# Kernel optimization log

Hardware: AMD Instinct MI355X
Metric: run time of the kernel (lower is better)

The kernel has to match this reference:

```python
import jax, jax.numpy as jnp
import numpy as np

H = 512   # hidden_size == mm_dim
C = 8     # chunks
R = 8     # rank
S = H // C  # chunk size = 64
OUT = 512 # output_dim of linear_merge
EPS = 1e-12

def _linear(x, w, b):
    # torch nn.Linear convention: w [out, in]
    return x @ w.T + b

def setup_inputs() -> dict:
    key = jax.random.key(0)
    ks = jax.random.split(key, 24)
    B, Lq, Lk, D = 8, 160, 160, 512
    s = 0.02
    inp = {
        'v': jax.random.normal(ks[0], (B, Lk, D), jnp.float32),
        'k': jax.random.normal(ks[1], (B, Lk, D), jnp.float32),
        'q': jax.random.normal(ks[2], (B, Lq, D), jnp.float32),
        # input projections
        'w_v': jax.random.normal(ks[3], (H, D)) * s, 'b_v': jnp.zeros((H,)),
        'w_k': jax.random.normal(ks[4], (H, D)) * s, 'b_k': jnp.zeros((H,)),
        'w_q': jax.random.normal(ks[5], (H, D)) * s, 'b_q': jnp.zeros((H,)),
        # Block: linear0 (applied to key), linear1 (applied to query)
        'w0': jax.random.normal(ks[6], (H, H)) * s, 'b0': jnp.zeros((H,)),
        'w1': jax.random.normal(ks[7], (H, H)) * s, 'b1': jnp.zeros((H,)),
        # per-chunk merge linears, stacked: [C, S*R, S]
        'wm0': jax.random.normal(ks[8], (C, S * R, S)) * s, 'bm0': jnp.zeros((C, S * R)),
        'wm1': jax.random.normal(ks[9], (C, S * R, S)) * s, 'bm1': jnp.zeros((C, S * R)),
        # Block linear_out: mm_dim -> 1
        'w_bo': jax.random.normal(ks[10], (1, H)) * s, 'b_bo': jnp.zeros((1,)),
        # linear_merge: hidden -> output_dim
        'w_m': jax.random.normal(ks[11], (OUT, H)) * s, 'b_m': jnp.zeros((OUT,)),
    }
    return inp

def _block_scores(kx, qx, w0, b0, w1, b1, wm0, bm0, wm1, bm1, w_bo, b_bo):
    # kx: [B,Lk,H] (block arg 0 = key), qx: [B,Lq,H] (block arg 1 = query)
    x0 = _linear(kx, w0, b0)                      # [B,Lk,H]
    x1 = _linear(qx, w1, b1)                      # [B,Lq,H]
    B_, Lk = x0.shape[0], x0.shape[1]
    Lq = x1.shape[1]
    x0c = x0.reshape(B_, Lk, C, S)
    x1c = x1.reshape(B_, Lq, C, S)
    # per-chunk merge projections to rank*size
    y0 = jnp.einsum('bkcs,cts->bkct', x0c, wm0) + bm0  # [B,Lk,C,R*S]
    y1 = jnp.einsum('bqcs,cts->bqct', x1c, wm1) + bm1  # [B,Lq,C,R*S]
    y0 = y0.reshape(B_, Lk, C, R, S)
    y1 = y1.reshape(B_, Lq, C, R, S)
    # elementwise product summed over rank, pairwise over (q,k)
    z = jnp.einsum('bqcrs,bkcrs->bqkcs', y1, y0)  # [B,Lq,Lk,C,S]
    # signed sqrt (power norm) then per-chunk L2 normalize
    z = jnp.sqrt(jax.nn.relu(z)) - jnp.sqrt(jax.nn.relu(-z))
    z = z / jnp.maximum(jnp.linalg.norm(z, axis=-1, keepdims=True), EPS)
    z = z.reshape(B_, Lq, Lk, C * S)
    return _linear(z, w_bo, b_bo).squeeze(-1)     # [B,Lq,Lk]

def reference(v, k, q, w_v, b_v, w_k, b_k, w_q, b_q, w0, b0, w1, b1,
              wm0, bm0, wm1, bm1, w_bo, b_bo, w_m, b_m):
    vv = _linear(v, w_v, b_v)   # [B,Lk,H]
    kk = _linear(k, w_k, b_k)   # [B,Lk,H]
    qq = _linear(q, w_q, b_q)   # [B,Lq,H]
    scores = _block_scores(kk, qq, w0, b0, w1, b1, wm0, bm0, wm1, bm1, w_bo, b_bo)
    att = jax.nn.softmax(scores, axis=-1)          # dropout = identity (eval)
    atted = jnp.einsum('bqk,bkh->bqh', att, vv)    # [B,Lq,H]
    B_ = atted.shape[0]
    # faithful to torch: transpose(1,2).contiguous().view(B,-1,H)
    atted = jnp.swapaxes(atted, 1, 2).reshape(B_, -1, H)
    out = _linear(atted, w_m, b_m)                 # [B,Lq,OUT]
    return jnp.squeeze(out)
```

## Files before the change

### kernel.cpp

```cpp
#include <hip/hip_runtime.h>
#include <hip/hip_bf16.h>

#define B_  8
#define LQ  160
#define LK  160

struct GOps {
    const float* A[3];
    const float* W[3];
    const float* Bi[3];
    float*       C[3];
};

__global__ __launch_bounds__(256) void gemm_f(GOps ops, int K)
{
    const int op = blockIdx.z;
    const float* __restrict__ A  = ops.A[op];
    const float* __restrict__ W  = ops.W[op];
    const float* __restrict__ Bi = ops.Bi[op];
    float* __restrict__       C  = ops.C[op];

    const int m0 = blockIdx.y << 6;
    const int n0 = blockIdx.x << 6;
    const int tid = threadIdx.x;
    const int tm  = tid >> 4;
    const int tn  = tid & 15;
    const int lr  = tid >> 2;
    const int lk4 = (tid & 3) << 2;

    __shared__ float As[16][64];
    __shared__ float Ws[16][64];

    float acc[4][4];
#pragma unroll
    for (int i = 0; i < 4; i++)
#pragma unroll
        for (int j = 0; j < 4; j++) acc[i][j] = 0.f;

    const float* Arow = A + (long)(m0 + lr) * 512 + lk4;
    const float* Wrow = W + (long)(n0 + lr) * K + lk4;
    float4 av = *(const float4*)(Arow);
    float4 wv = *(const float4*)(Wrow);

    for (int k0 = 0; k0 < K; k0 += 16) {
        __syncthreads();
        As[lk4 + 0][lr] = av.x; As[lk4 + 1][lr] = av.y;
        As[lk4 + 2][lr] = av.z; As[lk4 + 3][lr] = av.w;
        Ws[lk4 + 0][lr] = wv.x; Ws[lk4 + 1][lr] = wv.y;
        Ws[lk4 + 2][lr] = wv.z; Ws[lk4 + 3][lr] = wv.w;
        __syncthreads();
        if (k0 + 16 < K) {
            av = *(const float4*)(Arow + k0 + 16);
            wv = *(const float4*)(Wrow + k0 + 16);
        }
#pragma unroll
        for (int kk = 0; kk < 16; kk++) {
            const float4 a4 = *(const float4*)(&As[kk][tm << 2]);
            const float4 b4 = *(const float4*)(&Ws[kk][tn << 2]);
            const float aa[4] = {a4.x, a4.y, a4.z, a4.w};
            const float bb[4] = {b4.x, b4.y, b4.z, b4.w};
#pragma unroll
            for (int i = 0; i < 4; i++)
#pragma unroll
                for (int j = 0; j < 4; j++)
                    acc[i][j] = fmaf(aa[i], bb[j], acc[i][j]);
        }
    }

    const float4 bv = *(const float4*)(Bi + n0 + (tn << 2));
    const float bArr[4] = {bv.x, bv.y, bv.z, bv.w};

#pragma unroll
    for (int i = 0; i < 4; i++) {
        float4 vo;
        vo.x = acc[i][0] + bArr[0]; vo.y = acc[i][1] + bArr[1];
        vo.z = acc[i][2] + bArr[2]; vo.w = acc[i][3] + bArr[3];
        *(float4*)(C + (long)(m0 + (tm << 2) + i) * 512 + n0 + (tn << 2)) = vo;
    }
}

__global__ __launch_bounds__(256) void y_proj(
    const float* __restrict__ x0, const float* __restrict__ wm0, const float* __restrict__ bm0,
    const float* __restrict__ x1, const float* __restrict__ wm1, const float* __restrict__ bm1,
    float* __restrict__ y0t, float* __restrict__ y1p)
{
    const int z   = blockIdx.z;
    const bool is1 = z >= 8;
    const int c   = is1 ? z - 8 : z;
    const float* A  = (is1 ? x1 : x0) + (c << 6);
    const float* W  = (is1 ? wm1 : wm0) + c * 32768;
    const float* Bi = (is1 ? bm1 : bm0) + (c << 9);

    const int m0 = blockIdx.y << 6;
    const int bx  = blockIdx.x;
    const int n0 = bx << 6;
    const int s0 = bx << 3;
    const int tid = threadIdx.x;
    const int tm  = tid >> 4;
    const int tn  = tid & 15;
    const int lr  = tid >> 2;
    const int lk4 = (tid & 3) << 2;

    __shared__ float As[16][64];
    __shared__ float Ws[16][64];
    __shared__ float outT[4096];

    float acc[4][4];
#pragma unroll
    for (int i = 0; i < 4; i++)
#pragma unroll
        for (int j = 0; j < 4; j++) acc[i][j] = 0.f;

    const int wrow = is1 ? (n0 + lr) : (((lr & 7) << 6) + s0 + (lr >> 3));
    const float* Arow = A + (long)(m0 + lr) * 512 + lk4;
    const float* Wrow = W + (long)wrow * 64 + lk4;
    float4 av = *(const float4*)(Arow);
    float4 wv = *(const float4*)(Wrow);

    for (int k0 = 0; k0 < 64; k0 += 16) {
        __syncthreads();
        As[lk4 + 0][lr] = av.x; As[lk4 + 1][lr] = av.y;
        As[lk4 + 2][lr] = av.z; As[lk4 + 3][lr] = av.w;
        Ws[lk4 + 0][lr] = wv.x; Ws[lk4 + 1][lr] = wv.y;
        Ws[lk4 + 2][lr] = wv.z; Ws[lk4 + 3][lr] = wv.w;
        __syncthreads();
        if (k0 + 16 < 64) {
            av = *(const float4*)(Arow + k0 + 16);
            wv = *(const float4*)(Wrow + k0 + 16);
        }
#pragma unroll
        for (int kk = 0; kk < 16; kk++) {
            const float4 a4 = *(const float4*)(&As[kk][tm << 2]);
            const float4 b4 = *(const float4*)(&Ws[kk][tn << 2]);
            const float aa[4] = {a4.x, a4.y, a4.z, a4.w};
            const float bb[4] = {b4.x, b4.y, b4.z, b4.w};
#pragma unroll
            for (int i = 0; i < 4; i++)
#pragma unroll
                for (int j = 0; j < 4; j++)
                    acc[i][j] = fmaf(aa[i], bb[j], acc[i][j]);
        }
    }

    if (is1) {
        const float4 bv = *(const float4*)(Bi + n0 + (tn << 2));
        const float bArr[4] = {bv.x, bv.y, bv.z, bv.w};
#pragma unroll
        for (int i = 0; i < 4; i++) {
            const int m = m0 + (tm << 2) + i;
            float4 vo;
            vo.x = acc[i][0] + bArr[0]; vo.y = acc[i][1] + bArr[1];
            vo.z = acc[i][2] + bArr[2]; vo.w = acc[i][3] + bArr[3];
            *(float4*)(y1p + (long)m * 4096 + (c << 9) + n0 + (tn << 2)) = vo;
        }
    } else {
        float bArr[4];
#pragma unroll
        for (int j = 0; j < 4; j++) {
            const int ln = (tn << 2) + j;
            bArr[j] = Bi[((ln & 7) << 6) + s0 + (ln >> 3)];
        }
        __syncthreads();
#pragma unroll
        for (int i = 0; i < 4; i++) {
            const int k8 = (tm << 2) + i;
#pragma unroll
            for (int j = 0; j < 4; j++) {
                const int ln = (tn << 2) + j;
                outT[((ln >> 3) << 9) + (k8 << 3) + (ln & 7)] = acc[i][j] + bArr[j];
            }
        }
        __syncthreads();
#pragma unroll
        for (int p = 0; p < 4; p++) {
            const int s8  = (p << 1) + (tid >> 7);
            const int u4  = tid & 127;
            const int k8  = u4 >> 1;
            const int r   = (u4 & 1) << 2;
            const int m   = m0 + k8;
            const int bidx = m / 160;
            const int kmod = m - bidx * 160;
            const int s   = s0 + s8;
            float4* dst = (float4*)(y0t +
                (((long)(bidx * 8 + c) * 64 + s) * 160 + kmod) * 8 + r);
            *dst = *(const float4*)&outT[(s8 << 9) + (u4 << 2)];
        }
    }
}

__global__ __launch_bounds__(192) void score_partial(
    const float* __restrict__ y1p, const float* __restrict__ y0t,
    const float* __restrict__ wbo, float* __restrict__ scores_p)
{
    const int id = blockIdx.x;
    const int c  = id & 7;
    const int j  = id >> 3;
    const int b  = j / 40;
    const int q0 = (j - b * 40) << 2;
    const int tid = threadIdx.x;
    const int k   = tid;

    __shared__ float y1c[4][512];

    const long y1base = (long)(b * LQ + q0) * 4096 + (c << 9);
    for (int t = tid; t < 512; t += 192) {
        const int qq = t >> 7, e = t & 127;
        const float4 v =
            *(const float4*)(y1p + y1base + (long)qq * 4096 + (e << 2));
        const int r  = e >> 4;
        const int s4 = (e & 15) << 2;
        y1c[qq][(s4 + 0) * 8 + r] = v.x;
        y1c[qq][(s4 + 1) * 8 + r] = v.y;
        y1c[qq][(s4 + 2) * 8 + r] = v.z;
        y1c[qq][(s4 + 3) * 8 + r] = v.w;
    }
    __syncthreads();
    if (k >= LK) return;

    const float* wb  = wbo + (c << 6);
    const float* ybc = y0t + (((long)(b * 8 + c) * 64) * 160 + k) * 8;

    float num[4], den[4];
#pragma unroll
    for (int q = 0; q < 4; q++) { num[q] = 0.f; den[q] = 0.f; }

    float4 a0 = *(const float4*)(ybc);
    float4 a1 = *(const float4*)(ybc + 4);
    for (int s = 0; s < 64; s++) {
        const float a[8] = {a0.x, a0.y, a0.z, a0.w, a1.x, a1.y, a1.z, a1.w};
        const int sn = (s + 1) & 63;
        a0 = *(const float4*)(ybc + (long)sn * 1280);
        a1 = *(const float4*)(ybc + (long)sn * 1280 + 4);
        const float w = wb[s];
#pragma unroll
        for (int q = 0; q < 4; q++) {
            const float4 p0 = *(const float4*)(&y1c[q][s << 3]);
            const float4 p1 = *(const float4*)(&y1c[q][(s << 3) + 4]);
            float z = a[0] * p0.x;
            z = fmaf(a[1], p0.y, z); z = fmaf(a[2], p0.z, z); z = fmaf(a[3], p0.w, z);
            z = fmaf(a[4], p1.x, z); z = fmaf(a[5], p1.y, z);
            z = fmaf(a[6], p1.z, z); z = fmaf(a[7], p1.w, z);
            const float az = fabsf(z);
            num[q] = fmaf(copysignf(__builtin_amdgcn_sqrtf(az), z), w, num[q]);
            den[q] += az;
        }
    }
#pragma unroll
    for (int q = 0; q < 4; q++)
        scores_p[(((long)(b * LQ + q0 + q)) * 8 + c) * 160 + k] =
            num[q] / fmaxf(__builtin_amdgcn_sqrtf(den[q]), 1e-12f);
}

__global__ __launch_bounds__(256) void softmax_attv(
    const float* __restrict__ scores_p, const float* __restrict__ vv,
    float* __restrict__ attedT)
{
    const int b  = blockIdx.y;
    const int q0 = blockIdx.x << 2;
    const int tid = threadIdx.x;

    __shared__ float scs[4][160];
    __shared__ float invd[4];

    for (int t = tid; t < 640; t += 256) {
        const int q = t / 160;
        const int k = t - q * 160;
        const float* sp = scores_p + ((long)(b * LQ + q0 + q)) * 1280 + k;
        float s = 0.f;
#pragma unroll
        for (int c = 0; c < 8; c++) s += sp[c * 160];
        scs[q][k] = s;
    }
    __syncthreads();

    const int w    = tid >> 6;
    const int lane = tid & 63;
    {
        const int q = w;
        float m = -1e30f;
        for (int kk = lane; kk < LK; kk += 64) m = fmaxf(m, scs[q][kk]);
#pragma unroll
        for (int off = 32; off; off >>= 1) m = fmaxf(m, __shfl_xor(m, off, 64));
        float sum = 0.f;
        for (int kk = lane; kk < LK; kk += 64) {
            const float e = __expf(scs[q][kk] - m);
            scs[q][kk] = e;
            sum += e;
        }
#pragma unroll
        for (int off = 32; off; off >>= 1) sum += __shfl_xor(sum, off, 64);
        if (lane == 0) invd[q] = 1.f / sum;
    }
    __syncthreads();

    float acc[2][4] = {{0.f,0.f,0.f,0.f},{0.f,0.f,0.f,0.f}};
    const float* vb = vv + (long)b * (LK * 512);
    for (int kk = 0; kk < LK; kk++) {
        const float* vr = vb + kk * 512;
        const float p0 = scs[0][kk], p1 = scs[1][kk];
        const float p2 = scs[2][kk], p3 = scs[3][kk];
        const float v0 = vr[tid], v1 = vr[tid + 256];
        acc[0][0] = fmaf(p0, v0, acc[0][0]); acc[0][1] = fmaf(p1, v0, acc[0][1]);
        acc[0][2] = fmaf(p2, v0, acc[0][2]); acc[0][3] = fmaf(p3, v0, acc[0][3]);
        acc[1][0] = fmaf(p0, v1, acc[1][0]); acc[1][1] = fmaf(p1, v1, acc[1][1]);
        acc[1][2] = fmaf(p2, v1, acc[1][2]); acc[1][3] = fmaf(p3, v1, acc[1][3]);
    }
#pragma unroll
    for (int j = 0; j < 2; j++) {
        const int h = tid + (j << 8);
#pragma unroll
        for (int q = 0; q < 4; q++)
            attedT[((long)b * 512 + h) * 160 + q0 + q] = acc[j][q] * invd[q];
    }
}

extern "C" void kernel_launch(void* const* d_in, const int* in_sizes, int n_in,
                              void* d_out, int out_size, void* d_ws, size_t ws_size,
                              hipStream_t stream) {
    const float* v    = (const float*)d_in[0];
    const float* kin  = (const float*)d_in[1];
    const float* q    = (const float*)d_in[2];
    const float* w_v  = (const float*)d_in[3];
    const float* b_v  = (const float*)d_in[4];
    const float* w_k  = (const float*)d_in[5];
    const float* b_k  = (const float*)d_in[6];
    const float* w_q  = (const float*)d_in[7];
    const float* b_q  = (const float*)d_in[8];
    const float* w0   = (const float*)d_in[9];
    const float* b0   = (const float*)d_in[10];
    const float* w1   = (const float*)d_in[11];
    const float* b1   = (const float*)d_in[12];
    const float* wm0  = (const float*)d_in[13];
    const float* bm0  = (const float*)d_in[14];
    const float* wm1  = (const float*)d_in[15];
    const float* bm1  = (const float*)d_in[16];
    const float* w_bo = (const float*)d_in[17];
    (void)d_in[18];
    const float* w_m  = (const float*)d_in[19];
    const float* b_m  = (const float*)d_in[20];

    float* ws       = (float*)d_ws;
    float* vv       = ws;
    float* kk       = ws + 655360;
    float* qq       = ws + 1310720;
    float* x0       = ws + 1966080;
    float* x1       = ws + 2621440;
    float* y1p      = ws + 3276800;
    float* y0t      = ws + 8519680;
    float* attedT   = ws + 13762560;
    float* scores_p = ws + 655360;

    GOps oA;
    oA.A[0] = v;   oA.W[0] = w_v; oA.Bi[0] = b_v; oA.C[0] = vv;
    oA.A[1] = kin; oA.W[1] = w_k; oA.Bi[1] = b_k; oA.C[1] = kk;
    oA.A[2] = q;   oA.W[2] = w_q; oA.Bi[2] = b_q; oA.C[2] = qq;
    hipLaunchKernelGGL(gemm_f, dim3(8, 20, 3), dim3(256), 0, stream, oA, 512);

    GOps oB;
    oB.A[0] = kk; oB.W[0] = w0; oB.Bi[0] = b0; oB.C[0] = x0;
    oB.A[1] = qq; oB.W[1] = w1; oB.Bi[1] = b1; oB.C[1] = x1;
    oB.A[2] = nullptr; oB.W[2] = nullptr; oB.Bi[2] = nullptr; oB.C[2] = nullptr;
    hipLaunchKernelGGL(gemm_f, dim3(8, 20, 2), dim3(256), 0, stream, oB, 512);

    hipLaunchKernelGGL(y_proj, dim3(8, 20, 16), dim3(256), 0, stream,
                       x0, wm0, bm0, x1, wm1, bm1, y0t, y1p);

    hipLaunchKernelGGL(score_partial, dim3(2560), dim3(192), 0, stream,
                       y1p, y0t, w_bo, scores_p);

    hipLaunchKernelGGL(softmax_attv, dim3(40, 8), dim3(256), 0, stream,
                       scores_p, vv, attedT);

    GOps oF;
    oF.A[0] = attedT; oF.W[0] = w_m; oF.Bi[0] = b_m; oF.C[0] = (float*)d_out;
    oF.A[1] = nullptr; oF.W[1] = nullptr; oF.Bi[1] = nullptr; oF.C[1] = nullptr;
    oF.A[2] = nullptr; oF.W[2] = nullptr; oF.Bi[2] = nullptr; oF.C[2] = nullptr;
    hipLaunchKernelGGL(gemm_f, dim3(8, 20, 1), dim3(256), 0, stream, oF, 512);
}
```

Baseline: 296.7 us.

## Store y1 in s-major rank-interleaved layout and read it directly in score kernel

The y1 projection now uses the same permuted weight-row ordering as y0 and transposes through shared memory, so y1p is written with rank contiguous per chunk element (s*8+r). The score kernel then drops its shared-memory staging and transpose of y1 and reads the four query rows straight from global memory with wave-uniform addresses, which the compiler can turn into scalar loads. Out-of-range threads are clamped instead of returning early. This removes a barrier and the LDS transpose, but adds an extra LDS round-trip to the y1 projection epilogue and relies on scalar or cached global loads being fast.

Measured after the change: 298.8 us. About the same (+0.7%).

```diff
diff --git a/kernel.cpp b/kernel.cpp
--- a/kernel.cpp
+++ b/kernel.cpp
@@ -92,9 +92,7 @@
     const float* Bi = (is1 ? bm1 : bm0) + (c << 9);
 
     const int m0 = blockIdx.y << 6;
-    const int bx  = blockIdx.x;
-    const int n0 = bx << 6;
-    const int s0 = bx << 3;
+    const int s0 = blockIdx.x << 3;
     const int tid = threadIdx.x;
     const int tm  = tid >> 4;
     const int tn  = tid & 15;
@@ -111,7 +109,7 @@
 #pragma unroll
         for (int j = 0; j < 4; j++) acc[i][j] = 0.f;
 
-    const int wrow = is1 ? (n0 + lr) : (((lr & 7) << 6) + s0 + (lr >> 3));
+    const int wrow = ((lr & 7) << 6) + s0 + (lr >> 3);
     const float* Arow = A + (long)(m0 + lr) * 512 + lk4;
     const float* Wrow = W + (long)wrow * 64 + lk4;
     float4 av = *(const float4*)(Arow);
@@ -142,25 +140,33 @@
         }
     }
 
+    float bArr[4];
+#pragma unroll
+    for (int j = 0; j < 4; j++) {
+        const int ln = (tn << 2) + j;
+        bArr[j] = Bi[((ln & 7) << 6) + s0 + (ln >> 3)];
+    }
+    __syncthreads();
     if (is1) {
-        const float4 bv = *(const float4*)(Bi + n0 + (tn << 2));
-        const float bArr[4] = {bv.x, bv.y, bv.z, bv.w};
 #pragma unroll
         for (int i = 0; i < 4; i++) {
-            const int m = m0 + (tm << 2) + i;
-            float4 vo;
-            vo.x = acc[i][0] + bArr[0]; vo.y = acc[i][1] + bArr[1];
-            vo.z = acc[i][2] + bArr[2]; vo.w = acc[i][3] + bArr[3];
-            *(float4*)(y1p + (long)m * 4096 + (c << 9) + n0 + (tn << 2)) = vo;
+            const int m8 = (tm << 2) + i;
+#pragma unroll
+            for (int j = 0; j < 4; j++) {
+                const int ln = (tn << 2) + j;
+                outT[(m8 << 6) + ((ln >> 3) << 3) + (ln & 7)] = acc[i][j] + bArr[j];
+            }
+        }
+        __syncthreads();
+#pragma unroll
+        for (int p = 0; p < 4; p++) {
+            const int idx = tid + (p << 8);
+            const int m8  = idx >> 4;
+            const int f4  = idx & 15;
+            *(float4*)(y1p + (long)(m0 + m8) * 4096 + (c << 9) + (s0 << 3) + (f4 << 2))
+                = *(const float4*)&outT[idx << 2];
         }
     } else {
-        float bArr[4];
-#pragma unroll
-        for (int j = 0; j < 4; j++) {
-            const int ln = (tn << 2) + j;
-            bArr[j] = Bi[((ln & 7) << 6) + s0 + (ln >> 3)];
-        }
-        __syncthreads();
 #pragma unroll
         for (int i = 0; i < 4; i++) {
             const int k8 = (tm << 2) + i;
@@ -197,58 +203,76 @@
     const int j  = id >> 3;
     const int b  = j / 40;
     const int q0 = (j - b * 40) << 2;
-    const int tid = threadIdx.x;
-    const int k   = tid;
-
-    __shared__ float y1c[4][512];
-
-    const long y1base = (long)(b * LQ + q0) * 4096 + (c << 9);
-    for (int t = tid; t < 512; t += 192) {
-        const int qq = t >> 7, e = t & 127;
-        const float4 v =
-            *(const float4*)(y1p + y1base + (long)qq * 4096 + (e << 2));
-        const int r  = e >> 4;
-        const int s4 = (e & 15) << 2;
-        y1c[qq][(s4 + 0) * 8 + r] = v.x;
-        y1c[qq][(s4 + 1) * 8 + r] = v.y;
-        y1c[qq][(s4 + 2) * 8 + r] = v.z;
-        y1c[qq][(s4 + 3) * 8 + r] = v.w;
-    }
-    __syncthreads();
-    if (k >= LK) return;
-
-    const float* wb  = wbo + (c << 6);
-    const float* ybc = y0t + (((long)(b * 8 + c) * 64) * 160 + k) * 8;
-
-    float num[4], den[4];
-#pragma unroll
-    for (int q = 0; q < 4; q++) { num[q] = 0.f; den[q] = 0.f; }
+    const int k  = threadIdx.x;
+    const int kc = k < LK ? k : (LK - 1);
+
+    const float* wb = wbo + (c << 6);
+    const float* y1r0 = y1p + (long)(b * LQ + q0) * 4096 + (c << 9);
+    const float* y1r1 = y1r0 + 4096;
+    const float* y1r2 = y1r0 + 8192;
+    const float* y1r3 = y1r0 + 12288;
+    const float* ybc = y0t + (((long)(b * 8 + c) * 64) * 160 + kc) * 8;
+
+    float num[4] = {0.f, 0.f, 0.f, 0.f};
+    float den[4] = {0.f, 0.f, 0.f, 0.f};
 
     float4 a0 = *(const float4*)(ybc);
     float4 a1 = *(const float4*)(ybc + 4);
+#pragma unroll 2
     for (int s = 0; s < 64; s++) {
         const float a[8] = {a0.x, a0.y, a0.z, a0.w, a1.x, a1.y, a1.z, a1.w};
         const int sn = (s + 1) & 63;
         a0 = *(const float4*)(ybc + (long)sn * 1280);
         a1 = *(const float4*)(ybc + (long)sn * 1280 + 4);
         const float w = wb[s];
-#pragma unroll
-        for (int q = 0; q < 4; q++) {
-            const float4 p0 = *(const float4*)(&y1c[q][s << 3]);
-            const float4 p1 = *(const float4*)(&y1c[q][(s << 3) + 4]);
-            float z = a[0] * p0.x;
-            z = fmaf(a[1], p0.y, z); z = fmaf(a[2], p0.z, z); z = fmaf(a[3], p0.w, z);
-            z = fmaf(a[4], p1.x, z); z = fmaf(a[5], p1.y, z);
-            z = fmaf(a[6], p1.z, z); z = fmaf(a[7], p1.w, z);
-            const float az = fabsf(z);
-            num[q] = fmaf(copysignf(__builtin_amdgcn_sqrtf(az), z), w, num[q]);
-            den[q] += az;
-        }
-    }
-#pragma unroll
-    for (int q = 0; q < 4; q++)
-        scores_p[(((long)(b * LQ + q0 + q)) * 8 + c) * 160 + k] =
-            num[q] / fmaxf(__builtin_amdgcn_sqrtf(den[q]), 1e-12f);
+        const int o = s << 3;
+        {
+            float zv = a[0] * y1r0[o];
+            zv = fmaf(a[1], y1r0[o+1], zv); zv = fmaf(a[2], y1r0[o+2], zv);
+            zv = fmaf(a[3], y1r0[o+3], zv); zv = fmaf(a[4], y1r0[o+4], zv);
+            zv = fmaf(a[5], y1r0[o+5], zv); zv = fmaf(a[6], y1r0[o+6], zv);
+            zv = fmaf(a[7], y1r0[o+7], zv);
+            const float az = fabsf(zv);
+            num[0] = fmaf(copysignf(__builtin_amdgcn_sqrtf(az), zv), w, num[0]);
+            den[0] += az;
+        }
+        {
+            float zv = a[0] * y1r1[o];
+            zv = fmaf(a[1], y1r1[o+1], zv); zv = fmaf(a[2], y1r1[o+2], zv);
+            zv = fmaf(a[3], y1r1[o+3], zv); zv = fmaf(a[4], y1r1[o+4], zv);
+            zv = fmaf(a[5], y1r1[o+5], zv); zv = fmaf(a[6], y1r1[o+6], zv);
+            zv = fmaf(a[7], y1r1[o+7], zv);
+            const float az = fabsf(zv);
+            num[1] = fmaf(copysignf(__builtin_amdgcn_sqrtf(az), zv), w, num[1]);
+            den[1] += az;
+        }
+        {
+            float zv = a[0] * y1r2[o];
+            zv = fmaf(a[1], y1r2[o+1], zv); zv = fmaf(a[2], y1r2[o+2], zv);
+            zv = fmaf(a[3], y1r2[o+3], zv); zv = fmaf(a[4], y1r2[o+4], zv);
+            zv = fmaf(a[5], y1r2[o+5], zv); zv = fmaf(a[6], y1r2[o+6], zv);
+            zv = fmaf(a[7], y1r2[o+7], zv);
+            const float az = fabsf(zv);
+            num[2] = fmaf(copysignf(__builtin_amdgcn_sqrtf(az), zv), w, num[2]);
+            den[2] += az;
+        }
+        {
+            float zv = a[0] * y1r3[o];
+            zv = fmaf(a[1], y1r3[o+1], zv); zv = fmaf(a[2], y1r3[o+2], zv);
+            zv = fmaf(a[3], y1r3[o+3], zv); zv = fmaf(a[4], y1r3[o+4], zv);
+            zv = fmaf(a[5], y1r3[o+5], zv); zv = fmaf(a[6], y1r3[o+6], zv);
+            zv = fmaf(a[7], y1r3[o+7], zv);
+            const float az = fabsf(zv);
+            num[3] = fmaf(copysignf(__builtin_amdgcn_sqrtf(az), zv), w, num[3]);
+            den[3] += az;
+        }
+    }
+    if (k < LK) {
+#pragma unroll
+        for (int q = 0; q < 4; q++)
+            scores_p[(((long)(b * LQ + q0 + q)) * 8 + c) * 160 + k] =
+                num[q] / fmaxf(__builtin_amdgcn_sqrtf(den[q]), 1e-12f);
+    }
 }
 
 __global__ __launch_bounds__(256) void softmax_attv(
```
